# Kernel optimization log

Measured on AMD Instinct MI355X. Metric: run time of the kernel, lower is better.

Reference implementation:

```python
import jax, jax.numpy as jnp
import numpy as np

B, S, HID = 2, 2048, 2048
NH, HD = 16, 128
EPS = 1e-5


def setup_inputs() -> dict:
    key = jax.random.key(0)
    ks = jax.random.split(key, 6)
    std = 1.0 / np.sqrt(HID)
    x = jax.random.normal(ks[0], (B, S, HID), dtype=jnp.float32)
    Wq = jax.random.normal(ks[1], (HID, NH * HD), dtype=jnp.float32) * std
    Wk = jax.random.normal(ks[2], (HID, NH * HD), dtype=jnp.float32) * std
    Wv = jax.random.normal(ks[3], (HID, NH * HD), dtype=jnp.float32) * std
    Wo = jax.random.normal(ks[4], (NH * HD, HID), dtype=jnp.float32) * std
    rms_w = jnp.ones((HID,), dtype=jnp.float32)
    # RoPE tables: freqs_cis.real / .imag, shape [S, HD//2]
    inv_freq = 1.0 / (10000.0 ** (np.arange(0, HD, 2, dtype=np.float32) / HD))
    angles = jnp.asarray(np.arange(S, dtype=np.float32)[:, None] * inv_freq[None, :])
    cos = jnp.cos(angles)
    sin = jnp.sin(angles)
    return {"x": x, "rms_w": rms_w, "Wq": Wq, "Wk": Wk, "Wv": Wv, "Wo": Wo,
            "cos": cos, "sin": sin}


def _rmsnorm(x, w):
    var = jnp.mean(jnp.square(x), axis=-1, keepdims=True)
    return x * jax.lax.rsqrt(var + EPS) * w


def _rope(t, cos, sin):
    # t: [B, S, H, D]; cos/sin: [S, D/2]  (rotate-half RoPE)
    d2 = t.shape[-1] // 2
    t1, t2 = t[..., :d2], t[..., d2:]
    c = cos[None, :, None, :]
    s = sin[None, :, None, :]
    return jnp.concatenate([t1 * c - t2 * s, t2 * c + t1 * s], axis=-1)


def reference(x, rms_w, Wq, Wk, Wv, Wo, cos, sin):
    residual = x
    h = _rmsnorm(x, rms_w)
    q = (h @ Wq).reshape(B, S, NH, HD)
    k = (h @ Wk).reshape(B, S, NH, HD)
    v = (h @ Wv).reshape(B, S, NH, HD)
    q = _rope(q, cos, sin)
    k = _rope(k, cos, sin)
    # [B, H, S, D]
    q = q.transpose(0, 2, 1, 3)
    k = k.transpose(0, 2, 1, 3)
    v = v.transpose(0, 2, 1, 3)
    scale = 1.0 / jnp.sqrt(jnp.float32(HD))
    scores = jnp.einsum('bhqd,bhkd->bhqk', q, k) * scale
    causal = jnp.tril(jnp.ones((S, S), dtype=bool))
    scores = jnp.where(causal[None, None], scores, jnp.finfo(scores.dtype).min)
    probs = jax.nn.softmax(scores, axis=-1)
    attn = jnp.einsum('bhqk,bhkd->bhqd', probs, v)
    attn = attn.transpose(0, 2, 1, 3).reshape(B, S, NH * HD)
    out = attn @ Wo
    return (residual + out).astype(x.dtype)
```

## Files before the change

### kernel.cpp

```cpp
#include <hip/hip_runtime.h>

#define HID   2048
#define S_LEN 2048
#define NHEAD 16
#define HD    128
#define NKV   2048

typedef __attribute__((ext_vector_type(8))) short   short8;
typedef __attribute__((ext_vector_type(4))) float   floatx4;

__device__ __forceinline__ unsigned short f2bf(float f) {
    union { float f; unsigned u; } v; v.f = f;
    unsigned r = v.u + 0x7fffu + ((v.u >> 16) & 1u);
    return (unsigned short)(r >> 16);
}
__device__ __forceinline__ float bf2f(unsigned short h) {
    union { unsigned u; float f; } v; v.u = ((unsigned)h) << 16; return v.f;
}

__device__ __forceinline__ void async16(void* lds, const void* g) {
    __builtin_amdgcn_global_load_lds(
        (const __attribute__((address_space(1))) unsigned int*)g,
        (__attribute__((address_space(3))) unsigned int*)lds, 16, 0, 0);
}

__global__ __launch_bounds__(256) void rmsnorm_kernel(const float* __restrict__ x,
        const float* __restrict__ w, unsigned short* __restrict__ h) {
    const int row = blockIdx.x;
    const int t = threadIdx.x;
    const float* xr = x + (size_t)row * HID;
    float4 v0 = *(const float4*)(xr + t * 4);
    float4 v1 = *(const float4*)(xr + 1024 + t * 4);
    float ss = v0.x*v0.x + v0.y*v0.y + v0.z*v0.z + v0.w*v0.w
             + v1.x*v1.x + v1.y*v1.y + v1.z*v1.z + v1.w*v1.w;
    #pragma unroll
    for (int off = 1; off < 64; off <<= 1) ss += __shfl_xor(ss, off, 64);
    __shared__ float red[4];
    if ((t & 63) == 0) red[t >> 6] = ss;
    __syncthreads();
    float tot = red[0] + red[1] + red[2] + red[3];
    float inv = rsqrtf(tot * (1.0f / HID) + 1e-5f);
    float4 w0 = *(const float4*)(w + t * 4);
    float4 w1 = *(const float4*)(w + 1024 + t * 4);
    ushort4 o0, o1;
    o0.x = f2bf(v0.x * inv * w0.x); o0.y = f2bf(v0.y * inv * w0.y);
    o0.z = f2bf(v0.z * inv * w0.z); o0.w = f2bf(v0.w * inv * w0.w);
    o1.x = f2bf(v1.x * inv * w1.x); o1.y = f2bf(v1.y * inv * w1.y);
    o1.z = f2bf(v1.z * inv * w1.z); o1.w = f2bf(v1.w * inv * w1.w);
    *(ushort4*)(h + (size_t)row * HID + t * 4) = o0;
    *(ushort4*)(h + (size_t)row * HID + 1024 + t * 4) = o1;
}

__global__ __launch_bounds__(256) void wtrans_kernel(const float* __restrict__ Wq,
        const float* __restrict__ Wk, const float* __restrict__ Wv,
        const float* __restrict__ Wo,
        unsigned short* __restrict__ wt_qkv, unsigned short* __restrict__ wt_o) {
    __shared__ float tile[64][65];
    const int sel = blockIdx.z;
    const float* W = (sel == 0) ? Wq : (sel == 1) ? Wk : (sel == 2) ? Wv : Wo;
    const int n0 = blockIdx.x * 64, k0 = blockIdx.y * 64;
    const int t = threadIdx.x;
    const int col = t & 63, r4 = t >> 6;
    #pragma unroll
    for (int i = 0; i < 16; ++i) {
        int rr = r4 + i * 4;
        tile[rr][col] = W[(size_t)(k0 + rr) * NKV + n0 + col];
    }
    __syncthreads();
    #pragma unroll
    for (int i = 0; i < 16; ++i) {
        int rr = r4 + i * 4;
        unsigned short v = f2bf(tile[col][rr]);
        if (sel < 3) wt_qkv[((size_t)(sel * 2048 + n0 + rr)) * HID + k0 + col] = v;
        else         wt_o  [((size_t)(n0 + rr)) * HID + k0 + col] = v;
    }
}

__device__ __forceinline__ void gemm_body(const unsigned short* __restrict__ A,
        const unsigned short* __restrict__ Bt, int K, int rowBase, int colBase,
        unsigned short* As, unsigned short* Bs, floatx4 acc[4][4]) {
    const int t = threadIdx.x;
    const int lane = t & 63, w = t >> 6;
    const int wm = (w >> 1) * 64, wsel = w & 1;
    const int lr = lane & 15, quad = lane >> 4;
    #pragma unroll
    for (int mi = 0; mi < 4; ++mi)
        #pragma unroll
        for (int ni = 0; ni < 4; ++ni) {
            acc[mi][ni][0] = 0.f; acc[mi][ni][1] = 0.f;
            acc[mi][ni][2] = 0.f; acc[mi][ni][3] = 0.f;
        }
    for (int k0 = 0; k0 < K; k0 += 64) {
        __syncthreads();
        #pragma unroll
        for (int c = 0; c < 4; ++c) {
            int e = (c * 256 + t) * 8;
            int r = e >> 6;
            int chunk = ((e >> 3) & 7) ^ (r & 7);
            async16(As + e, A  + (size_t)(rowBase + r) * K + k0 + chunk * 8);
            async16(Bs + e, Bt + (size_t)(colBase + r) * K + k0 + chunk * 8);
        }
        __syncthreads();
        #pragma unroll
        for (int ks = 0; ks < 2; ++ks) {
            short8 af[4], bfr[4];
            int cp = (ks * 4 + quad) ^ (lr & 7);
            #pragma unroll
            for (int i = 0; i < 4; ++i)
                af[i] = *(const short8*)(As + (wm + i * 16 + lr) * 64 + cp * 8);
            #pragma unroll
            for (int i = 0; i < 4; ++i)
                bfr[i] = *(const short8*)(Bs + (i * 32 + wsel * 16 + lr) * 64 + cp * 8);
            #pragma unroll
            for (int mi = 0; mi < 4; ++mi)
                #pragma unroll
                for (int ni = 0; ni < 4; ++ni)
                    acc[mi][ni] = __builtin_amdgcn_mfma_f32_16x16x32_bf16(
                        af[mi], bfr[ni], acc[mi][ni], 0, 0, 0);
        }
    }
}

__global__ __launch_bounds__(256) void gemm_qkv_kernel(const unsigned short* __restrict__ h,
        const unsigned short* __restrict__ wt, const float* __restrict__ cosp,
        const float* __restrict__ sinp, unsigned short* __restrict__ qk,
        unsigned short* __restrict__ vT) {
    __shared__ __align__(16) unsigned short As[128 * 64];
    __shared__ __align__(16) unsigned short Bs[128 * 64];
    floatx4 acc[4][4];
    const int rowBase = blockIdx.y * 128, colBase = blockIdx.x * 128;
    gemm_body(h, wt, HID, rowBase, colBase, As, Bs, acc);
    const int t = threadIdx.x, lane = t & 63, w = t >> 6;
    const int wm = (w >> 1) * 64, wsel = w & 1;
    const int lr = lane & 15, quad = lane >> 4;
    const int sel = colBase >> 11;
    const int hh = (colBase >> 7) & 15;
    #pragma unroll
    for (int mi = 0; mi < 4; ++mi) {
        int row0 = rowBase + wm + mi * 16 + quad * 4;
        int b = row0 >> 11, s0 = row0 & 2047;
        if (sel < 2) {
            unsigned short* base = qk + (size_t)sel * 8388608
                                 + ((size_t)(b * NHEAD + hh) * S_LEN) * HD;
            #pragma unroll
            for (int ni = 0; ni < 2; ++ni) {
                int d = ni * 32 + wsel * 16 + lr;
                #pragma unroll
                for (int r = 0; r < 4; ++r) {
                    int s = s0 + r;
                    float c  = cosp[s * 64 + d];
                    float sn = sinp[s * 64 + d];
                    float v1 = acc[mi][ni][r], v2 = acc[mi][ni + 2][r];
                    base[(size_t)s * HD + d]      = f2bf(v1 * c - v2 * sn);
                    base[(size_t)s * HD + d + 64] = f2bf(v2 * c + v1 * sn);
                }
            }
        } else {
            #pragma unroll
            for (int ni = 0; ni < 4; ++ni) {
                int d = ni * 32 + wsel * 16 + lr;
                ushort4 pk;
                pk.x = f2bf(acc[mi][ni][0]); pk.y = f2bf(acc[mi][ni][1]);
                pk.z = f2bf(acc[mi][ni][2]); pk.w = f2bf(acc[mi][ni][3]);
                *(ushort4*)(vT + ((size_t)(b * NHEAD + hh) * HD + d) * S_LEN + s0) = pk;
            }
        }
    }
}

__global__ __launch_bounds__(256, 2) void attn_kernel(const unsigned short* __restrict__ q,
        const unsigned short* __restrict__ k, const unsigned short* __restrict__ vT,
        unsigned short* __restrict__ Opart, float* __restrict__ lpart) {
    __shared__ __align__(16) unsigned short Kd[2][64 * 128];
    __shared__ __align__(16) unsigned short Vd[2][128 * 64];
    __shared__ __align__(16) unsigned short Ps[4][32 * 64];

    const int id = blockIdx.x;
    const int bh   = id >> 4;
    const int j    = (id >> 1) & 7;
    const int role = id & 1;

    const int qtA = 15 - j, qtB = j;
    const int n1 = 16 - j;
    const int n2 = j + 1;
    const int segqt[2] = {qtA, qtB};
    const int segk0[2] = {role ? n1 : 0, role ? n2 : 0};
    const int seglen[2] = {n1, n2};

    const unsigned short* qb = q  + (size_t)bh * S_LEN * HD;
    const unsigned short* kb = k  + (size_t)bh * S_LEN * HD;
    const unsigned short* vb = vT + (size_t)bh * HD * S_LEN;
    const int t = threadIdx.x, lane = t & 63, w = t >> 6;
    const int lr = lane & 15, quad = lane >> 4;
    const float SC = 0.1275174855f;

    short8 qf[2][4];
    floatx4 o[2][8];
    float rs[2][4];
    #pragma unroll
    for (int mi = 0; mi < 2; ++mi) {
        #pragma unroll
        for (int i = 0; i < 8; ++i) { o[mi][i][0]=0.f; o[mi][i][1]=0.f; o[mi][i][2]=0.f; o[mi][i][3]=0.f; }
        rs[mi][0]=0.f; rs[mi][1]=0.f; rs[mi][2]=0.f; rs[mi][3]=0.f;
    }

    auto loadq = [&](int qt) {
        #pragma unroll
        for (int mi = 0; mi < 2; ++mi) {
            int qrow = qt * 128 + mi * 64 + w * 16 + lr;
            #pragma unroll
            for (int ks = 0; ks < 4; ++ks) {
                short8 raw = *(const short8*)(qb + (size_t)qrow * HD + ks * 32 + quad * 8);
                #pragma unroll
                for (int jj = 0; jj < 8; ++jj)
                    qf[mi][ks][jj] = (short)f2bf(bf2f((unsigned short)raw[jj]) * SC);
            }
        }
    };

    auto stage = [&](int kt2, int buf) {
        unsigned short* Kb = &Kd[buf][0];
        unsigned short* Vb = &Vd[buf][0];
        #pragma unroll
        for (int c = 0; c < 4; ++c) {
            int e = (c * 256 + t) * 8;
            int kr = e >> 7;
            int kch = ((e >> 3) & 15) ^ (kr & 15);
            async16(Kb + e, kb + (size_t)(kt2 * 64 + kr) * HD + kch * 8);
            int vr = e >> 6;
            int vch = ((e >> 3) & 7) ^ (vr & 7);
            async16(Vb + e, vb + (size_t)vr * S_LEN + kt2 * 64 + vch * 8);
        }
    };

    auto tilework = [&](int qt, int kt, int buf, bool maskf) {
        const unsigned short* Ksb = &Kd[buf][0];
        const unsigned short* Vsb = &Vd[buf][0];
        floatx4 sc[2][4];
        #pragma unroll
        for (int mi = 0; mi < 2; ++mi)
            #pragma unroll
            for (int ni = 0; ni < 4; ++ni) { sc[mi][ni][0]=0.f; sc[mi][ni][1]=0.f; sc[mi][ni][2]=0.f; sc[mi][ni][3]=0.f; }
        #pragma unroll
        for (int ks = 0; ks < 4; ++ks) {
            #pragma unroll
            for (int ni = 0; ni < 4; ++ni) {
                int row = ni * 16 + lr;
                int cp = (ks * 4 + quad) ^ (lr & 15);
                short8 kf = *(const short8*)(Ksb + row * 128 + cp * 8);
                sc[0][ni] = __builtin_amdgcn_mfma_f32_16x16x32_bf16(qf[0][ks], kf, sc[0][ni], 0, 0, 0);
                sc[1][ni] = __builtin_amdgcn_mfma_f32_16x16x32_bf16(qf[1][ks], kf, sc[1][ni], 0, 0, 0);
            }
        }
        #pragma unroll
        for (int mi = 0; mi < 2; ++mi) {
            int row_out = qt * 128 + mi * 64 + w * 16 + quad * 4;
            #pragma unroll
            for (int ni = 0; ni < 4; ++ni) {
                int key = kt * 64 + ni * 16 + lr;
                #pragma unroll
                for (int r = 0; r < 4; ++r) {
                    float p = exp2f(sc[mi][ni][r]);
                    if (maskf && key > row_out + r) p = 0.f;
                    rs[mi][r] += p;
                    int prow = mi * 16 + quad * 4 + r;
                    int chunk = (ni * 2 + (lr >> 3)) ^ (prow & 7);
                    Ps[w][prow * 64 + chunk * 8 + (lr & 7)] =
                        (unsigned short)(__float_as_uint(p) >> 16);
                }
            }
        }
        #pragma unroll
        for (int ks2 = 0; ks2 < 2; ++ks2) {
            int pcp = (ks2 * 4 + quad) ^ (lr & 7);
            short8 pa0 = *(const short8*)(&Ps[w][(lr) * 64 + pcp * 8]);
            short8 pa1 = *(const short8*)(&Ps[w][(16 + lr) * 64 + pcp * 8]);
            #pragma unroll
            for (int nt = 0; nt < 8; ++nt) {
                int row = nt * 16 + lr;
                int vcp = (ks2 * 4 + quad) ^ (lr & 7);
                short8 vf = *(const short8*)(Vsb + row * 64 + vcp * 8);
                o[0][nt] = __builtin_amdgcn_mfma_f32_16x16x32_bf16(pa0, vf, o[0][nt], 0, 0, 0);
                o[1][nt] = __builtin_amdgcn_mfma_f32_16x16x32_bf16(pa1, vf, o[1][nt], 0, 0, 0);
            }
        }
    };

    auto flushseg = [&](int qt) {
        unsigned short* ob = Opart + (size_t)role * 8388608
                           + ((size_t)(bh * 16 + qt) * 128) * 128;
        float* lb = lpart + role * 65536 + (bh * 16 + qt) * 128;
        #pragma unroll
        for (int mi = 0; mi < 2; ++mi) {
            int qrow0 = mi * 64 + w * 16 + quad * 4;
            #pragma unroll
            for (int r = 0; r < 4; ++r) {
                float s2 = rs[mi][r];
                #pragma unroll
                for (int off = 1; off < 16; off <<= 1) s2 += __shfl_xor(s2, off, 64);
                if (lr == 0) lb[qrow0 + r] = s2;
            }
            #pragma unroll
            for (int nt = 0; nt < 8; ++nt) {
                int col = nt * 16 + lr;
                #pragma unroll
                for (int r = 0; r < 4; ++r)
                    ob[(size_t)(qrow0 + r) * 128 + col] = f2bf(o[mi][nt][r]);
            }
            #pragma unroll
            for (int i = 0; i < 8; ++i) { o[mi][i][0]=0.f; o[mi][i][1]=0.f; o[mi][i][2]=0.f; o[mi][i][3]=0.f; }
            rs[mi][0]=0.f; rs[mi][1]=0.f; rs[mi][2]=0.f; rs[mi][3]=0.f;
        }
    };

    stage(segk0[0], 0);
    int g = 0;
    for (int s = 0; s < 2; ++s) {
        loadq(segqt[s]);
        const int qt = segqt[s], k0 = segk0[s], len = seglen[s];
        for (int i = 0; i < len; ++i, ++g) {
            __syncthreads();
            int ns = s, nidx = i + 1;
            if (nidx == len) { ns = s + 1; nidx = 0; }
            if (ns < 2) stage(segk0[ns] + nidx, (g + 1) & 1);
            int kt = k0 + i;
            tilework(qt, kt, g & 1, kt >= 2 * qt);
        }
        flushseg(qt);
    }
}

__global__ __launch_bounds__(256) void combine_kernel(const unsigned short* __restrict__ Opart,
        const float* __restrict__ lpart, unsigned short* __restrict__ attn) {
    const int T = blockIdx.x;
    const int bh = T >> 4, qt = T & 15;
    const int b = bh >> 4, hh = bh & 15;
    const int t = threadIdx.x;
    const int qrow = t >> 1, half = t & 1;
    float rl = 1.0f / (lpart[T * 128 + qrow] + lpart[65536 + T * 128 + qrow]);
    const unsigned short* pa = Opart + ((size_t)T * 128 + qrow) * 128 + half * 64;
    const unsigned short* pb = Opart + 8388608 + ((size_t)T * 128 + qrow) * 128 + half * 64;
    unsigned short* po = attn + ((size_t)(b * S_LEN + qt * 128 + qrow)) * NKV + hh * HD + half * 64;
    #pragma unroll
    for (int c = 0; c < 8; ++c) {
        short8 a8 = *(const short8*)(pa + c * 8);
        short8 b8 = *(const short8*)(pb + c * 8);
        short8 o8;
        #pragma unroll
        for (int jj = 0; jj < 8; ++jj)
            o8[jj] = (short)f2bf((bf2f((unsigned short)a8[jj]) + bf2f((unsigned short)b8[jj])) * rl);
        *(short8*)(po + c * 8) = o8;
    }
}

__global__ __launch_bounds__(256) void gemm_out_kernel(const unsigned short* __restrict__ attn,
        const unsigned short* __restrict__ wto, const float* __restrict__ x,
        float* __restrict__ out) {
    __shared__ __align__(16) unsigned short As[128 * 64];
    __shared__ __align__(16) unsigned short Bs[128 * 64];
    floatx4 acc[4][4];
    const int rowBase = blockIdx.y * 128, colBase = blockIdx.x * 128;
    gemm_body(attn, wto, NKV, rowBase, colBase, As, Bs, acc);
    const int t = threadIdx.x, lane = t & 63, w = t >> 6;
    const int wm = (w >> 1) * 64, wsel = w & 1;
    const int lr = lane & 15, quad = lane >> 4;
    #pragma unroll
    for (int mi = 0; mi < 4; ++mi) {
        int row0 = rowBase + wm + mi * 16 + quad * 4;
        #pragma unroll
        for (int ni = 0; ni < 4; ++ni) {
            int col = colBase + ni * 32 + wsel * 16 + lr;
            #pragma unroll
            for (int r = 0; r < 4; ++r) {
                size_t off = (size_t)(row0 + r) * HID + col;
                out[off] = acc[mi][ni][r] + x[off];
            }
        }
    }
}

extern "C" void kernel_launch(void* const* d_in, const int* in_sizes, int n_in,
                              void* d_out, int out_size, void* d_ws, size_t ws_size,
                              hipStream_t stream) {
    const float* x     = (const float*)d_in[0];
    const float* rms_w = (const float*)d_in[1];
    const float* Wq    = (const float*)d_in[2];
    const float* Wk    = (const float*)d_in[3];
    const float* Wv    = (const float*)d_in[4];
    const float* Wo    = (const float*)d_in[5];
    const float* cosp  = (const float*)d_in[6];
    const float* sinp  = (const float*)d_in[7];
    float* out = (float*)d_out;

    unsigned short* ws   = (unsigned short*)d_ws;
    unsigned short* h    = ws;
    unsigned short* wtq  = ws + 8388608;
    unsigned short* wto  = ws + 20971520;
    unsigned short* qk   = ws + 25165824;
    unsigned short* vT   = ws + 41943040;
    unsigned short* attn = ws + 50331648;
    unsigned short* Opart = ws;
    float* lpart = (float*)(ws + 16777216);

    rmsnorm_kernel<<<4096, 256, 0, stream>>>(x, rms_w, h);
    wtrans_kernel<<<dim3(32, 32, 4), 256, 0, stream>>>(Wq, Wk, Wv, Wo, wtq, wto);
    gemm_qkv_kernel<<<dim3(48, 32), 256, 0, stream>>>(h, wtq, cosp, sinp, qk, vT);
    attn_kernel<<<512, 256, 0, stream>>>(qk, qk + 8388608, vT, Opart, lpart);
    combine_kernel<<<512, 256, 0, stream>>>(Opart, lpart, attn);
    gemm_out_kernel<<<dim3(16, 32), 256, 0, stream>>>(attn, wto, x, out);
}
```

Before: 417.9 us.

## Load K/V fragments directly from global into registers, dropping LDS staging

Replaces the double-buffered LDS staging of K and V tiles (async global-to-LDS loads plus __syncthreads) with per-wave direct global loads of MFMA fragments into registers. The next K tile is prefetched during the current softmax/PV step, and V is loaded in two halves. This removes block-wide barriers and LDS traffic, but each of the 4 waves now reads the same K/V data from global/L2 separately. It also raises register pressure (kf[4][4], vf[8]), which may hurt the 2-block occupancy target.

```diff
diff --git a/kernel.cpp b/kernel.cpp
--- a/kernel.cpp
+++ b/kernel.cpp
@@ -171,8 +171,6 @@
 __global__ __launch_bounds__(256, 2) void attn_kernel(const unsigned short* __restrict__ q,
         const unsigned short* __restrict__ k, const unsigned short* __restrict__ vT,
         unsigned short* __restrict__ Opart, float* __restrict__ lpart) {
-    __shared__ __align__(16) unsigned short Kd[2][64 * 128];
-    __shared__ __align__(16) unsigned short Vd[2][128 * 64];
     __shared__ __align__(16) unsigned short Ps[4][32 * 64];
 
     const int id = blockIdx.x;
@@ -195,6 +193,8 @@
     const float SC = 0.1275174855f;
 
     short8 qf[2][4];
+    short8 kf[4][4];
+    short8 vf[8];
     floatx4 o[2][8];
     float rs[2][4];
     #pragma unroll
@@ -218,72 +218,20 @@
         }
     };
 
-    auto stage = [&](int kt2, int buf) {
-        unsigned short* Kb = &Kd[buf][0];
-        unsigned short* Vb = &Vd[buf][0];
-        #pragma unroll
-        for (int c = 0; c < 4; ++c) {
-            int e = (c * 256 + t) * 8;
-            int kr = e >> 7;
-            int kch = ((e >> 3) & 15) ^ (kr & 15);
-            async16(Kb + e, kb + (size_t)(kt2 * 64 + kr) * HD + kch * 8);
-            int vr = e >> 6;
-            int vch = ((e >> 3) & 7) ^ (vr & 7);
-            async16(Vb + e, vb + (size_t)vr * S_LEN + kt2 * 64 + vch * 8);
-        }
+    auto loadK = [&](int kt2) {
+        #pragma unroll
+        for (int ks = 0; ks < 4; ++ks)
+            #pragma unroll
+            for (int ni = 0; ni < 4; ++ni)
+                kf[ks][ni] = *(const short8*)(kb
+                    + (size_t)(kt2 * 64 + ni * 16 + lr) * HD + ks * 32 + quad * 8);
     };
 
-    auto tilework = [&](int qt, int kt, int buf, bool maskf) {
-        const unsigned short* Ksb = &Kd[buf][0];
-        const unsigned short* Vsb = &Vd[buf][0];
-        floatx4 sc[2][4];
-        #pragma unroll
-        for (int mi = 0; mi < 2; ++mi)
-            #pragma unroll
-            for (int ni = 0; ni < 4; ++ni) { sc[mi][ni][0]=0.f; sc[mi][ni][1]=0.f; sc[mi][ni][2]=0.f; sc[mi][ni][3]=0.f; }
-        #pragma unroll
-        for (int ks = 0; ks < 4; ++ks) {
-            #pragma unroll
-            for (int ni = 0; ni < 4; ++ni) {
-                int row = ni * 16 + lr;
-                int cp = (ks * 4 + quad) ^ (lr & 15);
-                short8 kf = *(const short8*)(Ksb + row * 128 + cp * 8);
-                sc[0][ni] = __builtin_amdgcn_mfma_f32_16x16x32_bf16(qf[0][ks], kf, sc[0][ni], 0, 0, 0);
-                sc[1][ni] = __builtin_amdgcn_mfma_f32_16x16x32_bf16(qf[1][ks], kf, sc[1][ni], 0, 0, 0);
-            }
-        }
-        #pragma unroll
-        for (int mi = 0; mi < 2; ++mi) {
-            int row_out = qt * 128 + mi * 64 + w * 16 + quad * 4;
-            #pragma unroll
-            for (int ni = 0; ni < 4; ++ni) {
-                int key = kt * 64 + ni * 16 + lr;
-                #pragma unroll
-                for (int r = 0; r < 4; ++r) {
-                    float p = exp2f(sc[mi][ni][r]);
-                    if (maskf && key > row_out + r) p = 0.f;
-                    rs[mi][r] += p;
-                    int prow = mi * 16 + quad * 4 + r;
-                    int chunk = (ni * 2 + (lr >> 3)) ^ (prow & 7);
-                    Ps[w][prow * 64 + chunk * 8 + (lr & 7)] =
-                        (unsigned short)(__float_as_uint(p) >> 16);
-                }
-            }
-        }
-        #pragma unroll
-        for (int ks2 = 0; ks2 < 2; ++ks2) {
-            int pcp = (ks2 * 4 + quad) ^ (lr & 7);
-            short8 pa0 = *(const short8*)(&Ps[w][(lr) * 64 + pcp * 8]);
-            short8 pa1 = *(const short8*)(&Ps[w][(16 + lr) * 64 + pcp * 8]);
-            #pragma unroll
-            for (int nt = 0; nt < 8; ++nt) {
-                int row = nt * 16 + lr;
-                int vcp = (ks2 * 4 + quad) ^ (lr & 7);
-                short8 vf = *(const short8*)(Vsb + row * 64 + vcp * 8);
-                o[0][nt] = __builtin_amdgcn_mfma_f32_16x16x32_bf16(pa0, vf, o[0][nt], 0, 0, 0);
-                o[1][nt] = __builtin_amdgcn_mfma_f32_16x16x32_bf16(pa1, vf, o[1][nt], 0, 0, 0);
-            }
-        }
+    auto loadV = [&](int kt2, int half) {
+        #pragma unroll
+        for (int nt = 0; nt < 8; ++nt)
+            vf[nt] = *(const short8*)(vb
+                + (size_t)(nt * 16 + lr) * S_LEN + kt2 * 64 + half * 32 + quad * 8);
     };
 
     auto flushseg = [&](int qt) {
@@ -313,18 +261,62 @@
         }
     };
 
-    stage(segk0[0], 0);
-    int g = 0;
+    loadK(segk0[0]);
     for (int s = 0; s < 2; ++s) {
         loadq(segqt[s]);
         const int qt = segqt[s], k0 = segk0[s], len = seglen[s];
-        for (int i = 0; i < len; ++i, ++g) {
-            __syncthreads();
-            int ns = s, nidx = i + 1;
-            if (nidx == len) { ns = s + 1; nidx = 0; }
-            if (ns < 2) stage(segk0[ns] + nidx, (g + 1) & 1);
-            int kt = k0 + i;
-            tilework(qt, kt, g & 1, kt >= 2 * qt);
+        for (int i = 0; i < len; ++i) {
+            const int kt = k0 + i;
+            loadV(kt, 0);
+            floatx4 sc[2][4];
+            #pragma unroll
+            for (int mi = 0; mi < 2; ++mi)
+                #pragma unroll
+                for (int ni = 0; ni < 4; ++ni) { sc[mi][ni][0]=0.f; sc[mi][ni][1]=0.f; sc[mi][ni][2]=0.f; sc[mi][ni][3]=0.f; }
+            #pragma unroll
+            for (int ks = 0; ks < 4; ++ks)
+                #pragma unroll
+                for (int ni = 0; ni < 4; ++ni) {
+                    sc[0][ni] = __builtin_amdgcn_mfma_f32_16x16x32_bf16(qf[0][ks], kf[ks][ni], sc[0][ni], 0, 0, 0);
+                    sc[1][ni] = __builtin_amdgcn_mfma_f32_16x16x32_bf16(qf[1][ks], kf[ks][ni], sc[1][ni], 0, 0, 0);
+                }
+            {
+                int ns = s, nidx = i + 1;
+                if (nidx == len) { ns = s + 1; nidx = 0; }
+                int nk = (ns < 2) ? (segk0[ns & 1] + nidx) : kt;
+                loadK(nk);
+            }
+            const bool maskf = (kt >= 2 * qt);
+            #pragma unroll
+            for (int mi = 0; mi < 2; ++mi) {
+                int row_out = qt * 128 + mi * 64 + w * 16 + quad * 4;
+                #pragma unroll
+                for (int ni = 0; ni < 4; ++ni) {
+                    int key = kt * 64 + ni * 16 + lr;
+                    #pragma unroll
+                    for (int r = 0; r < 4; ++r) {
+                        float p = exp2f(sc[mi][ni][r]);
+                        if (maskf && key > row_out + r) p = 0.f;
+                        rs[mi][r] += p;
+                        int prow = mi * 16 + quad * 4 + r;
+                        int chunk = (ni * 2 + (lr >> 3)) ^ (prow & 7);
+                        Ps[w][prow * 64 + chunk * 8 + (lr & 7)] =
+                            (unsigned short)(__float_as_uint(p) >> 16);
+                    }
+                }
+            }
+            #pragma unroll
+            for (int ks2 = 0; ks2 < 2; ++ks2) {
+                int pcp = (ks2 * 4 + quad) ^ (lr & 7);
+                short8 pa0 = *(const short8*)(&Ps[w][(lr) * 64 + pcp * 8]);
+                short8 pa1 = *(const short8*)(&Ps[w][(16 + lr) * 64 + pcp * 8]);
+                #pragma unroll
+                for (int nt = 0; nt < 8; ++nt) {
+                    o[0][nt] = __builtin_amdgcn_mfma_f32_16x16x32_bf16(pa0, vf[nt], o[0][nt], 0, 0, 0);
+                    o[1][nt] = __builtin_amdgcn_mfma_f32_16x16x32_bf16(pa1, vf[nt], o[1][nt], 0, 0, 0);
+                }
+                if (ks2 == 0) loadV(kt, 1);
+            }
         }
         flushseg(qt);
     }
```

Measured after the change: 508.9 us. 1.22x slower.

## Halve attention tile sizes to 64-query by 32-key blocks for more occupancy

Applied to the files above, without the earlier changes.

Restructures the attention kernel from 128-query by 64-key tiles to 64-query by 32-key tiles. The grid doubles to 1024 blocks, each pairing query tile 31-j with tile j and splitting the key range between two roles. LDS and register use per block shrink so launch bounds can request 4 blocks per CU instead of 2. The combine kernel is adjusted to the new 64-row partitions. The gain in occupancy and parallelism comes at the cost of less data reuse per K/V load and more barriers per unit of work.

```diff
diff --git a/kernel.cpp b/kernel.cpp
--- a/kernel.cpp
+++ b/kernel.cpp
@@ -168,24 +168,19 @@
     }
 }
 
-__global__ __launch_bounds__(256, 2) void attn_kernel(const unsigned short* __restrict__ q,
+__global__ __launch_bounds__(256, 4) void attn_kernel(const unsigned short* __restrict__ q,
         const unsigned short* __restrict__ k, const unsigned short* __restrict__ vT,
         unsigned short* __restrict__ Opart, float* __restrict__ lpart) {
-    __shared__ __align__(16) unsigned short Kd[2][64 * 128];
-    __shared__ __align__(16) unsigned short Vd[2][128 * 64];
-    __shared__ __align__(16) unsigned short Ps[4][32 * 64];
+    __shared__ __align__(16) unsigned short Kd[2][32 * 128];
+    __shared__ __align__(16) unsigned short Vd[2][128 * 32];
+    __shared__ __align__(16) unsigned short Ps[4][16 * 32];
 
     const int id = blockIdx.x;
-    const int bh   = id >> 4;
-    const int j    = (id >> 1) & 7;
+    const int bh   = id >> 5;
+    const int j    = (id >> 1) & 15;
     const int role = id & 1;
 
-    const int qtA = 15 - j, qtB = j;
-    const int n1 = 16 - j;
-    const int n2 = j + 1;
-    const int segqt[2] = {qtA, qtB};
-    const int segk0[2] = {role ? n1 : 0, role ? n2 : 0};
-    const int seglen[2] = {n1, n2};
+    const int segqt[2] = {31 - j, j};
 
     const unsigned short* qb = q  + (size_t)bh * S_LEN * HD;
     const unsigned short* kb = k  + (size_t)bh * S_LEN * HD;
@@ -194,27 +189,20 @@
     const int lr = lane & 15, quad = lane >> 4;
     const float SC = 0.1275174855f;
 
-    short8 qf[2][4];
-    floatx4 o[2][8];
-    float rs[2][4];
-    #pragma unroll
-    for (int mi = 0; mi < 2; ++mi) {
-        #pragma unroll
-        for (int i = 0; i < 8; ++i) { o[mi][i][0]=0.f; o[mi][i][1]=0.f; o[mi][i][2]=0.f; o[mi][i][3]=0.f; }
-        rs[mi][0]=0.f; rs[mi][1]=0.f; rs[mi][2]=0.f; rs[mi][3]=0.f;
-    }
+    short8 qf[4];
+    floatx4 o[8];
+    float rs[4] = {0.f, 0.f, 0.f, 0.f};
+    #pragma unroll
+    for (int i = 0; i < 8; ++i) { o[i][0]=0.f; o[i][1]=0.f; o[i][2]=0.f; o[i][3]=0.f; }
 
     auto loadq = [&](int qt) {
-        #pragma unroll
-        for (int mi = 0; mi < 2; ++mi) {
-            int qrow = qt * 128 + mi * 64 + w * 16 + lr;
-            #pragma unroll
-            for (int ks = 0; ks < 4; ++ks) {
-                short8 raw = *(const short8*)(qb + (size_t)qrow * HD + ks * 32 + quad * 8);
-                #pragma unroll
-                for (int jj = 0; jj < 8; ++jj)
-                    qf[mi][ks][jj] = (short)f2bf(bf2f((unsigned short)raw[jj]) * SC);
-            }
+        int qrow = qt * 64 + w * 16 + lr;
+        #pragma unroll
+        for (int ks = 0; ks < 4; ++ks) {
+            short8 raw = *(const short8*)(qb + (size_t)qrow * HD + ks * 32 + quad * 8);
+            #pragma unroll
+            for (int jj = 0; jj < 8; ++jj)
+                qf[ks][jj] = (short)f2bf(bf2f((unsigned short)raw[jj]) * SC);
         }
     };
 
@@ -222,107 +210,97 @@
         unsigned short* Kb = &Kd[buf][0];
         unsigned short* Vb = &Vd[buf][0];
         #pragma unroll
-        for (int c = 0; c < 4; ++c) {
+        for (int c = 0; c < 2; ++c) {
             int e = (c * 256 + t) * 8;
             int kr = e >> 7;
             int kch = ((e >> 3) & 15) ^ (kr & 15);
-            async16(Kb + e, kb + (size_t)(kt2 * 64 + kr) * HD + kch * 8);
-            int vr = e >> 6;
-            int vch = ((e >> 3) & 7) ^ (vr & 7);
-            async16(Vb + e, vb + (size_t)vr * S_LEN + kt2 * 64 + vch * 8);
+            async16(Kb + e, kb + (size_t)(kt2 * 32 + kr) * HD + kch * 8);
+            int vr = e >> 5;
+            int vch = ((e >> 3) & 3) ^ (vr & 3);
+            async16(Vb + e, vb + (size_t)vr * S_LEN + kt2 * 32 + vch * 8);
         }
     };
 
     auto tilework = [&](int qt, int kt, int buf, bool maskf) {
         const unsigned short* Ksb = &Kd[buf][0];
         const unsigned short* Vsb = &Vd[buf][0];
-        floatx4 sc[2][4];
-        #pragma unroll
-        for (int mi = 0; mi < 2; ++mi)
-            #pragma unroll
-            for (int ni = 0; ni < 4; ++ni) { sc[mi][ni][0]=0.f; sc[mi][ni][1]=0.f; sc[mi][ni][2]=0.f; sc[mi][ni][3]=0.f; }
-        #pragma unroll
-        for (int ks = 0; ks < 4; ++ks) {
-            #pragma unroll
-            for (int ni = 0; ni < 4; ++ni) {
+        floatx4 sc[2];
+        sc[0][0]=0.f; sc[0][1]=0.f; sc[0][2]=0.f; sc[0][3]=0.f;
+        sc[1][0]=0.f; sc[1][1]=0.f; sc[1][2]=0.f; sc[1][3]=0.f;
+        #pragma unroll
+        for (int ks = 0; ks < 4; ++ks)
+            #pragma unroll
+            for (int ni = 0; ni < 2; ++ni) {
                 int row = ni * 16 + lr;
-                int cp = (ks * 4 + quad) ^ (lr & 15);
+                int cp = (ks * 4 + quad) ^ (row & 15);
                 short8 kf = *(const short8*)(Ksb + row * 128 + cp * 8);
-                sc[0][ni] = __builtin_amdgcn_mfma_f32_16x16x32_bf16(qf[0][ks], kf, sc[0][ni], 0, 0, 0);
-                sc[1][ni] = __builtin_amdgcn_mfma_f32_16x16x32_bf16(qf[1][ks], kf, sc[1][ni], 0, 0, 0);
-            }
-        }
-        #pragma unroll
-        for (int mi = 0; mi < 2; ++mi) {
-            int row_out = qt * 128 + mi * 64 + w * 16 + quad * 4;
-            #pragma unroll
-            for (int ni = 0; ni < 4; ++ni) {
-                int key = kt * 64 + ni * 16 + lr;
-                #pragma unroll
-                for (int r = 0; r < 4; ++r) {
-                    float p = exp2f(sc[mi][ni][r]);
-                    if (maskf && key > row_out + r) p = 0.f;
-                    rs[mi][r] += p;
-                    int prow = mi * 16 + quad * 4 + r;
-                    int chunk = (ni * 2 + (lr >> 3)) ^ (prow & 7);
-                    Ps[w][prow * 64 + chunk * 8 + (lr & 7)] =
-                        (unsigned short)(__float_as_uint(p) >> 16);
-                }
-            }
-        }
-        #pragma unroll
-        for (int ks2 = 0; ks2 < 2; ++ks2) {
-            int pcp = (ks2 * 4 + quad) ^ (lr & 7);
-            short8 pa0 = *(const short8*)(&Ps[w][(lr) * 64 + pcp * 8]);
-            short8 pa1 = *(const short8*)(&Ps[w][(16 + lr) * 64 + pcp * 8]);
-            #pragma unroll
-            for (int nt = 0; nt < 8; ++nt) {
-                int row = nt * 16 + lr;
-                int vcp = (ks2 * 4 + quad) ^ (lr & 7);
-                short8 vf = *(const short8*)(Vsb + row * 64 + vcp * 8);
-                o[0][nt] = __builtin_amdgcn_mfma_f32_16x16x32_bf16(pa0, vf, o[0][nt], 0, 0, 0);
-                o[1][nt] = __builtin_amdgcn_mfma_f32_16x16x32_bf16(pa1, vf, o[1][nt], 0, 0, 0);
-            }
+                sc[ni] = __builtin_amdgcn_mfma_f32_16x16x32_bf16(qf[ks], kf, sc[ni], 0, 0, 0);
+            }
+        const int row_out = qt * 64 + w * 16 + quad * 4;
+        #pragma unroll
+        for (int ni = 0; ni < 2; ++ni) {
+            int key = kt * 32 + ni * 16 + lr;
+            #pragma unroll
+            for (int r = 0; r < 4; ++r) {
+                float p = exp2f(sc[ni][r]);
+                if (maskf && key > row_out + r) p = 0.f;
+                rs[r] += p;
+                int prow = quad * 4 + r;
+                int chunk = (ni * 2 + (lr >> 3)) ^ (prow & 3);
+                Ps[w][prow * 32 + chunk * 8 + (lr & 7)] =
+                    (unsigned short)(__float_as_uint(p) >> 16);
+            }
+        }
+        short8 pa = *(const short8*)(&Ps[w][lr * 32 + (quad ^ (lr & 3)) * 8]);
+        #pragma unroll
+        for (int nt = 0; nt < 8; ++nt) {
+            int vrow = nt * 16 + lr;
+            int vcp = quad ^ (vrow & 3);
+            short8 vf = *(const short8*)(Vsb + vrow * 32 + vcp * 8);
+            o[nt] = __builtin_amdgcn_mfma_f32_16x16x32_bf16(pa, vf, o[nt], 0, 0, 0);
         }
     };
 
     auto flushseg = [&](int qt) {
         unsigned short* ob = Opart + (size_t)role * 8388608
-                           + ((size_t)(bh * 16 + qt) * 128) * 128;
-        float* lb = lpart + role * 65536 + (bh * 16 + qt) * 128;
-        #pragma unroll
-        for (int mi = 0; mi < 2; ++mi) {
-            int qrow0 = mi * 64 + w * 16 + quad * 4;
-            #pragma unroll
-            for (int r = 0; r < 4; ++r) {
-                float s2 = rs[mi][r];
-                #pragma unroll
-                for (int off = 1; off < 16; off <<= 1) s2 += __shfl_xor(s2, off, 64);
-                if (lr == 0) lb[qrow0 + r] = s2;
-            }
-            #pragma unroll
-            for (int nt = 0; nt < 8; ++nt) {
-                int col = nt * 16 + lr;
-                #pragma unroll
-                for (int r = 0; r < 4; ++r)
-                    ob[(size_t)(qrow0 + r) * 128 + col] = f2bf(o[mi][nt][r]);
-            }
-            #pragma unroll
-            for (int i = 0; i < 8; ++i) { o[mi][i][0]=0.f; o[mi][i][1]=0.f; o[mi][i][2]=0.f; o[mi][i][3]=0.f; }
-            rs[mi][0]=0.f; rs[mi][1]=0.f; rs[mi][2]=0.f; rs[mi][3]=0.f;
+                           + ((size_t)(bh * 32 + qt) * 64) * 128;
+        float* lb = lpart + role * 65536 + (bh * 32 + qt) * 64;
+        int qrow0 = w * 16 + quad * 4;
+        #pragma unroll
+        for (int r = 0; r < 4; ++r) {
+            float s2 = rs[r];
+            #pragma unroll
+            for (int off = 1; off < 16; off <<= 1) s2 += __shfl_xor(s2, off, 64);
+            if (lr == 0) lb[qrow0 + r] = s2;
+            rs[r] = 0.f;
+        }
+        #pragma unroll
+        for (int nt = 0; nt < 8; ++nt) {
+            int col = nt * 16 + lr;
+            #pragma unroll
+            for (int r = 0; r < 4; ++r)
+                ob[(size_t)(qrow0 + r) * 128 + col] = f2bf(o[nt][r]);
+            o[nt][0]=0.f; o[nt][1]=0.f; o[nt][2]=0.f; o[nt][3]=0.f;
         }
     };
 
-    stage(segk0[0], 0);
+    {
+        int qt0 = segqt[0];
+        stage(role * (qt0 + 1), 0);
+    }
     int g = 0;
     for (int s = 0; s < 2; ++s) {
-        loadq(segqt[s]);
-        const int qt = segqt[s], k0 = segk0[s], len = seglen[s];
+        const int qt = segqt[s];
+        const int k0 = role * (qt + 1), len = qt + 1;
+        loadq(qt);
         for (int i = 0; i < len; ++i, ++g) {
             __syncthreads();
             int ns = s, nidx = i + 1;
             if (nidx == len) { ns = s + 1; nidx = 0; }
-            if (ns < 2) stage(segk0[ns] + nidx, (g + 1) & 1);
+            if (ns < 2) {
+                int nqt = segqt[ns];
+                stage(role * (nqt + 1) + nidx, (g + 1) & 1);
+            }
             int kt = k0 + i;
             tilework(qt, kt, g & 1, kt >= 2 * qt);
         }
@@ -333,16 +311,17 @@
 __global__ __launch_bounds__(256) void combine_kernel(const unsigned short* __restrict__ Opart,
         const float* __restrict__ lpart, unsigned short* __restrict__ attn) {
     const int T = blockIdx.x;
-    const int bh = T >> 4, qt = T & 15;
+    const int bh = T >> 5, qt = T & 31;
     const int b = bh >> 4, hh = bh & 15;
     const int t = threadIdx.x;
-    const int qrow = t >> 1, half = t & 1;
-    float rl = 1.0f / (lpart[T * 128 + qrow] + lpart[65536 + T * 128 + qrow]);
-    const unsigned short* pa = Opart + ((size_t)T * 128 + qrow) * 128 + half * 64;
-    const unsigned short* pb = Opart + 8388608 + ((size_t)T * 128 + qrow) * 128 + half * 64;
-    unsigned short* po = attn + ((size_t)(b * S_LEN + qt * 128 + qrow)) * NKV + hh * HD + half * 64;
-    #pragma unroll
-    for (int c = 0; c < 8; ++c) {
+    const int qrow = t >> 2, quarter = t & 3;
+    float rl = 1.0f / (lpart[T * 64 + qrow] + lpart[65536 + T * 64 + qrow]);
+    const unsigned short* pa = Opart + ((size_t)T * 64 + qrow) * 128 + quarter * 32;
+    const unsigned short* pb = pa + 8388608;
+    unsigned short* po = attn + ((size_t)(b * S_LEN + qt * 64 + qrow)) * NKV
+                       + hh * HD + quarter * 32;
+    #pragma unroll
+    for (int c = 0; c < 4; ++c) {
         short8 a8 = *(const short8*)(pa + c * 8);
         short8 b8 = *(const short8*)(pb + c * 8);
         short8 o8;
@@ -405,7 +384,7 @@
     rmsnorm_kernel<<<4096, 256, 0, stream>>>(x, rms_w, h);
     wtrans_kernel<<<dim3(32, 32, 4), 256, 0, stream>>>(Wq, Wk, Wv, Wo, wtq, wto);
     gemm_qkv_kernel<<<dim3(48, 32), 256, 0, stream>>>(h, wtq, cosp, sinp, qk, vT);
-    attn_kernel<<<512, 256, 0, stream>>>(qk, qk + 8388608, vT, Opart, lpart);
-    combine_kernel<<<512, 256, 0, stream>>>(Opart, lpart, attn);
+    attn_kernel<<<1024, 256, 0, stream>>>(qk, qk + 8388608, vT, Opart, lpart);
+    combine_kernel<<<1024, 256, 0, stream>>>(Opart, lpart, attn);
     gemm_out_kernel<<<dim3(16, 32), 256, 0, stream>>>(attn, wto, x, out);
 }
```

After: 407.5 us. -2.5%, faster.

## Split attention per query tile with 32-key tiles and longest-first scheduling

Applied to the files above, without the earlier changes.

The attention kernel no longer pairs two query tiles per block. Each block now handles one query tile and one half of its causal key range, giving 1024 blocks dispatched longest-first. The key/value tile shrinks from 64 to 32 keys, which halves the LDS footprint and allows three blocks per CU via launch bounds. The aim is better occupancy and load balance. The cost is twice as many barriers and stage steps per key, with less MFMA work between each sync.

```diff
diff --git a/kernel.cpp b/kernel.cpp
--- a/kernel.cpp
+++ b/kernel.cpp
@@ -168,24 +168,21 @@
     }
 }
 
-__global__ __launch_bounds__(256, 2) void attn_kernel(const unsigned short* __restrict__ q,
+__global__ __launch_bounds__(256, 3) void attn_kernel(const unsigned short* __restrict__ q,
         const unsigned short* __restrict__ k, const unsigned short* __restrict__ vT,
         unsigned short* __restrict__ Opart, float* __restrict__ lpart) {
-    __shared__ __align__(16) unsigned short Kd[2][64 * 128];
-    __shared__ __align__(16) unsigned short Vd[2][128 * 64];
-    __shared__ __align__(16) unsigned short Ps[4][32 * 64];
+    __shared__ __align__(16) unsigned short Kd[2][32 * 128];
+    __shared__ __align__(16) unsigned short Vd[2][128 * 32];
+    __shared__ __align__(16) unsigned short Ps[4][32 * 32];
 
     const int id = blockIdx.x;
-    const int bh   = id >> 4;
-    const int j    = (id >> 1) & 7;
+    const int qrank = id >> 6;
+    const int qt   = 15 - qrank;
+    const int bh   = (id >> 1) & 31;
     const int role = id & 1;
 
-    const int qtA = 15 - j, qtB = j;
-    const int n1 = 16 - j;
-    const int n2 = j + 1;
-    const int segqt[2] = {qtA, qtB};
-    const int segk0[2] = {role ? n1 : 0, role ? n2 : 0};
-    const int seglen[2] = {n1, n2};
+    const int nIters = 2 * qt + 2;
+    const int k0 = role * nIters;
 
     const unsigned short* qb = q  + (size_t)bh * S_LEN * HD;
     const unsigned short* kb = k  + (size_t)bh * S_LEN * HD;
@@ -204,129 +201,109 @@
         rs[mi][0]=0.f; rs[mi][1]=0.f; rs[mi][2]=0.f; rs[mi][3]=0.f;
     }
 
-    auto loadq = [&](int qt) {
-        #pragma unroll
-        for (int mi = 0; mi < 2; ++mi) {
-            int qrow = qt * 128 + mi * 64 + w * 16 + lr;
-            #pragma unroll
-            for (int ks = 0; ks < 4; ++ks) {
-                short8 raw = *(const short8*)(qb + (size_t)qrow * HD + ks * 32 + quad * 8);
-                #pragma unroll
-                for (int jj = 0; jj < 8; ++jj)
-                    qf[mi][ks][jj] = (short)f2bf(bf2f((unsigned short)raw[jj]) * SC);
-            }
-        }
-    };
+    #pragma unroll
+    for (int mi = 0; mi < 2; ++mi) {
+        int qrow = qt * 128 + mi * 64 + w * 16 + lr;
+        #pragma unroll
+        for (int ks = 0; ks < 4; ++ks) {
+            short8 raw = *(const short8*)(qb + (size_t)qrow * HD + ks * 32 + quad * 8);
+            #pragma unroll
+            for (int jj = 0; jj < 8; ++jj)
+                qf[mi][ks][jj] = (short)f2bf(bf2f((unsigned short)raw[jj]) * SC);
+        }
+    }
 
     auto stage = [&](int kt2, int buf) {
         unsigned short* Kb = &Kd[buf][0];
         unsigned short* Vb = &Vd[buf][0];
         #pragma unroll
-        for (int c = 0; c < 4; ++c) {
+        for (int c = 0; c < 2; ++c) {
             int e = (c * 256 + t) * 8;
             int kr = e >> 7;
             int kch = ((e >> 3) & 15) ^ (kr & 15);
-            async16(Kb + e, kb + (size_t)(kt2 * 64 + kr) * HD + kch * 8);
-            int vr = e >> 6;
-            int vch = ((e >> 3) & 7) ^ (vr & 7);
-            async16(Vb + e, vb + (size_t)vr * S_LEN + kt2 * 64 + vch * 8);
+            async16(Kb + e, kb + (size_t)(kt2 * 32 + kr) * HD + kch * 8);
+            int vr = e >> 5;
+            int vch = ((e >> 3) & 3) ^ (vr & 3);
+            async16(Vb + e, vb + (size_t)vr * S_LEN + kt2 * 32 + vch * 8);
         }
     };
 
-    auto tilework = [&](int qt, int kt, int buf, bool maskf) {
-        const unsigned short* Ksb = &Kd[buf][0];
-        const unsigned short* Vsb = &Vd[buf][0];
-        floatx4 sc[2][4];
+    stage(k0, 0);
+    for (int i = 0; i < nIters; ++i) {
+        __syncthreads();
+        if (i + 1 < nIters) stage(k0 + i + 1, (i + 1) & 1);
+        const int kt = k0 + i;
+        const bool maskf = (kt >= 4 * qt);
+        const unsigned short* Ksb = &Kd[i & 1][0];
+        const unsigned short* Vsb = &Vd[i & 1][0];
+
+        floatx4 sc[2][2];
         #pragma unroll
         for (int mi = 0; mi < 2; ++mi)
             #pragma unroll
-            for (int ni = 0; ni < 4; ++ni) { sc[mi][ni][0]=0.f; sc[mi][ni][1]=0.f; sc[mi][ni][2]=0.f; sc[mi][ni][3]=0.f; }
-        #pragma unroll
-        for (int ks = 0; ks < 4; ++ks) {
-            #pragma unroll
-            for (int ni = 0; ni < 4; ++ni) {
+            for (int ni = 0; ni < 2; ++ni) { sc[mi][ni][0]=0.f; sc[mi][ni][1]=0.f; sc[mi][ni][2]=0.f; sc[mi][ni][3]=0.f; }
+        #pragma unroll
+        for (int ks = 0; ks < 4; ++ks)
+            #pragma unroll
+            for (int ni = 0; ni < 2; ++ni) {
                 int row = ni * 16 + lr;
-                int cp = (ks * 4 + quad) ^ (lr & 15);
+                int cp = (ks * 4 + quad) ^ (row & 15);
                 short8 kf = *(const short8*)(Ksb + row * 128 + cp * 8);
                 sc[0][ni] = __builtin_amdgcn_mfma_f32_16x16x32_bf16(qf[0][ks], kf, sc[0][ni], 0, 0, 0);
                 sc[1][ni] = __builtin_amdgcn_mfma_f32_16x16x32_bf16(qf[1][ks], kf, sc[1][ni], 0, 0, 0);
             }
-        }
+
         #pragma unroll
         for (int mi = 0; mi < 2; ++mi) {
             int row_out = qt * 128 + mi * 64 + w * 16 + quad * 4;
             #pragma unroll
-            for (int ni = 0; ni < 4; ++ni) {
-                int key = kt * 64 + ni * 16 + lr;
+            for (int ni = 0; ni < 2; ++ni) {
+                int key = kt * 32 + ni * 16 + lr;
                 #pragma unroll
                 for (int r = 0; r < 4; ++r) {
                     float p = exp2f(sc[mi][ni][r]);
                     if (maskf && key > row_out + r) p = 0.f;
                     rs[mi][r] += p;
                     int prow = mi * 16 + quad * 4 + r;
-                    int chunk = (ni * 2 + (lr >> 3)) ^ (prow & 7);
-                    Ps[w][prow * 64 + chunk * 8 + (lr & 7)] =
+                    int chunk = (ni * 2 + (lr >> 3)) ^ (prow & 3);
+                    Ps[w][prow * 32 + chunk * 8 + (lr & 7)] =
                         (unsigned short)(__float_as_uint(p) >> 16);
                 }
             }
         }
-        #pragma unroll
-        for (int ks2 = 0; ks2 < 2; ++ks2) {
-            int pcp = (ks2 * 4 + quad) ^ (lr & 7);
-            short8 pa0 = *(const short8*)(&Ps[w][(lr) * 64 + pcp * 8]);
-            short8 pa1 = *(const short8*)(&Ps[w][(16 + lr) * 64 + pcp * 8]);
-            #pragma unroll
-            for (int nt = 0; nt < 8; ++nt) {
-                int row = nt * 16 + lr;
-                int vcp = (ks2 * 4 + quad) ^ (lr & 7);
-                short8 vf = *(const short8*)(Vsb + row * 64 + vcp * 8);
-                o[0][nt] = __builtin_amdgcn_mfma_f32_16x16x32_bf16(pa0, vf, o[0][nt], 0, 0, 0);
-                o[1][nt] = __builtin_amdgcn_mfma_f32_16x16x32_bf16(pa1, vf, o[1][nt], 0, 0, 0);
-            }
-        }
-    };
-
-    auto flushseg = [&](int qt) {
-        unsigned short* ob = Opart + (size_t)role * 8388608
-                           + ((size_t)(bh * 16 + qt) * 128) * 128;
-        float* lb = lpart + role * 65536 + (bh * 16 + qt) * 128;
-        #pragma unroll
-        for (int mi = 0; mi < 2; ++mi) {
-            int qrow0 = mi * 64 + w * 16 + quad * 4;
-            #pragma unroll
-            for (int r = 0; r < 4; ++r) {
-                float s2 = rs[mi][r];
-                #pragma unroll
-                for (int off = 1; off < 16; off <<= 1) s2 += __shfl_xor(s2, off, 64);
-                if (lr == 0) lb[qrow0 + r] = s2;
-            }
-            #pragma unroll
-            for (int nt = 0; nt < 8; ++nt) {
-                int col = nt * 16 + lr;
-                #pragma unroll
-                for (int r = 0; r < 4; ++r)
-                    ob[(size_t)(qrow0 + r) * 128 + col] = f2bf(o[mi][nt][r]);
-            }
-            #pragma unroll
-            for (int i = 0; i < 8; ++i) { o[mi][i][0]=0.f; o[mi][i][1]=0.f; o[mi][i][2]=0.f; o[mi][i][3]=0.f; }
-            rs[mi][0]=0.f; rs[mi][1]=0.f; rs[mi][2]=0.f; rs[mi][3]=0.f;
-        }
-    };
-
-    stage(segk0[0], 0);
-    int g = 0;
-    for (int s = 0; s < 2; ++s) {
-        loadq(segqt[s]);
-        const int qt = segqt[s], k0 = segk0[s], len = seglen[s];
-        for (int i = 0; i < len; ++i, ++g) {
-            __syncthreads();
-            int ns = s, nidx = i + 1;
-            if (nidx == len) { ns = s + 1; nidx = 0; }
-            if (ns < 2) stage(segk0[ns] + nidx, (g + 1) & 1);
-            int kt = k0 + i;
-            tilework(qt, kt, g & 1, kt >= 2 * qt);
-        }
-        flushseg(qt);
+
+        int pslot = (quad ^ (lr & 3)) * 8;
+        short8 pa0 = *(const short8*)(&Ps[w][lr * 32 + pslot]);
+        short8 pa1 = *(const short8*)(&Ps[w][(16 + lr) * 32 + pslot]);
+        #pragma unroll
+        for (int nt = 0; nt < 8; ++nt) {
+            int vrow = nt * 16 + lr;
+            short8 vf = *(const short8*)(Vsb + vrow * 32 + pslot);
+            o[0][nt] = __builtin_amdgcn_mfma_f32_16x16x32_bf16(pa0, vf, o[0][nt], 0, 0, 0);
+            o[1][nt] = __builtin_amdgcn_mfma_f32_16x16x32_bf16(pa1, vf, o[1][nt], 0, 0, 0);
+        }
+    }
+
+    unsigned short* ob = Opart + (size_t)role * 8388608
+                       + ((size_t)(bh * 16 + qt) * 128) * 128;
+    float* lb = lpart + role * 65536 + (bh * 16 + qt) * 128;
+    #pragma unroll
+    for (int mi = 0; mi < 2; ++mi) {
+        int qrow0 = mi * 64 + w * 16 + quad * 4;
+        #pragma unroll
+        for (int r = 0; r < 4; ++r) {
+            float s2 = rs[mi][r];
+            #pragma unroll
+            for (int off = 1; off < 16; off <<= 1) s2 += __shfl_xor(s2, off, 64);
+            if (lr == 0) lb[qrow0 + r] = s2;
+        }
+        #pragma unroll
+        for (int nt = 0; nt < 8; ++nt) {
+            int col = nt * 16 + lr;
+            #pragma unroll
+            for (int r = 0; r < 4; ++r)
+                ob[(size_t)(qrow0 + r) * 128 + col] = f2bf(o[mi][nt][r]);
+        }
     }
 }
 
@@ -339,7 +316,7 @@
     const int qrow = t >> 1, half = t & 1;
     float rl = 1.0f / (lpart[T * 128 + qrow] + lpart[65536 + T * 128 + qrow]);
     const unsigned short* pa = Opart + ((size_t)T * 128 + qrow) * 128 + half * 64;
-    const unsigned short* pb = Opart + 8388608 + ((size_t)T * 128 + qrow) * 128 + half * 64;
+    const unsigned short* pb = pa + 8388608;
     unsigned short* po = attn + ((size_t)(b * S_LEN + qt * 128 + qrow)) * NKV + hh * HD + half * 64;
     #pragma unroll
     for (int c = 0; c < 8; ++c) {
@@ -405,7 +382,7 @@
     rmsnorm_kernel<<<4096, 256, 0, stream>>>(x, rms_w, h);
     wtrans_kernel<<<dim3(32, 32, 4), 256, 0, stream>>>(Wq, Wk, Wv, Wo, wtq, wto);
     gemm_qkv_kernel<<<dim3(48, 32), 256, 0, stream>>>(h, wtq, cosp, sinp, qk, vT);
-    attn_kernel<<<512, 256, 0, stream>>>(qk, qk + 8388608, vT, Opart, lpart);
+    attn_kernel<<<1024, 256, 0, stream>>>(qk, qk + 8388608, vT, Opart, lpart);
     combine_kernel<<<512, 256, 0, stream>>>(Opart, lpart, attn);
     gemm_out_kernel<<<dim3(16, 32), 256, 0, stream>>>(attn, wto, x, out);
 }
```

New measurement: 416.9 us. No clear change (-0.2%).
